# Performance work log

Measured on AMD Instinct MI355X. Metric: run time of the kernel, lower is better.

The kernel has to match this reference:

```python
import jax, jax.numpy as jnp
import numpy as np

R = 8
EPS = 1e-08


def diff_x(t, r):
    # t: (B,C,H,W), running cumsum along H -> windowed sum along H
    left = t[:, :, r:2 * r + 1]
    middle = t[:, :, 2 * r + 1:] - t[:, :, :-2 * r - 1]
    right = t[:, :, -1:] - t[:, :, -2 * r - 1:-r - 1]
    return jnp.concatenate([left, middle, right], axis=2)


def diff_y(t, r):
    left = t[:, :, :, r:2 * r + 1]
    middle = t[:, :, :, 2 * r + 1:] - t[:, :, :, :-2 * r - 1]
    right = t[:, :, :, -1:] - t[:, :, :, -2 * r - 1:-r - 1]
    return jnp.concatenate([left, middle, right], axis=3)


def box_filter(x, r):
    return diff_y(diff_x(jnp.cumsum(x, axis=2), r).cumsum(axis=3), r)


def bilinear_align_corners(x, H, W):
    # x: (B,C,h,w) -> (B,C,H,W), matching F.interpolate(mode='bilinear', align_corners=True)
    h, w = x.shape[2], x.shape[3]
    ys = jnp.linspace(0.0, h - 1.0, H, dtype=x.dtype)
    xs = jnp.linspace(0.0, w - 1.0, W, dtype=x.dtype)
    y0 = jnp.clip(jnp.floor(ys).astype(jnp.int32), 0, h - 1)
    x0 = jnp.clip(jnp.floor(xs).astype(jnp.int32), 0, w - 1)
    y1 = jnp.clip(y0 + 1, 0, h - 1)
    x1 = jnp.clip(x0 + 1, 0, w - 1)
    wy = (ys - y0.astype(x.dtype))[:, None]   # (H,1)
    wx = (xs - x0.astype(x.dtype))[None, :]   # (1,W)
    v00 = x[:, :, y0[:, None], x0[None, :]]
    v01 = x[:, :, y0[:, None], x1[None, :]]
    v10 = x[:, :, y1[:, None], x0[None, :]]
    v11 = x[:, :, y1[:, None], x1[None, :]]
    top = v00 * (1 - wx) + v01 * wx
    bot = v10 * (1 - wx) + v11 * wx
    return top * (1 - wy) + bot * wy


def setup_inputs() -> dict:
    key = jax.random.key(0)
    k1, k2, k3 = jax.random.split(key, 3)
    lr_x = jax.random.uniform(k1, (4, 3, 512, 512), dtype=jnp.float32)
    lr_y = jax.random.uniform(k2, (4, 3, 512, 512), dtype=jnp.float32)
    hr_x = jax.random.uniform(k3, (4, 3, 2048, 2048), dtype=jnp.float32)
    return {"lr_x": lr_x, "lr_y": lr_y, "hr_x": hr_x}


def reference(lr_x, lr_y, hr_x):
    _, _, h_lr, w_lr = lr_x.shape
    _, _, h_hr, w_hr = hr_x.shape
    N = box_filter(jnp.ones((1, 1, h_lr, w_lr), dtype=lr_x.dtype), R)
    mean_x = box_filter(lr_x, R) / N
    mean_y = box_filter(lr_y, R) / N
    cov_xy = box_filter(lr_x * lr_y, R) / N - mean_x * mean_y
    var_x = box_filter(lr_x * lr_x, R) / N - mean_x * mean_x
    A = cov_xy / (var_x + EPS)
    b = mean_y - A * mean_x
    mean_A = bilinear_align_corners(A, h_hr, w_hr)
    mean_b = bilinear_align_corners(b, h_hr, w_hr)
    return mean_A * hr_x + mean_b
```

## Files before the change

### kernel.cpp

```cpp
#include <hip/hip_runtime.h>

#define RR 8
#define TILE 32
#define EXT (TILE + 2 * RR)

__global__ __launch_bounds__(1024) void k_ab(
    const float* __restrict__ lrx, const float* __restrict__ lry,
    float* __restrict__ Aout, float* __restrict__ Bout, int H, int W) {
  __shared__ float sx[EXT][EXT];
  __shared__ float sy[EXT][EXT];
  __shared__ float hx[EXT][TILE];
  __shared__ float hy[EXT][TILE];
  __shared__ float hxy[EXT][TILE];
  __shared__ float hxx[EXT][TILE];

  const int bc = blockIdx.z;
  const size_t plane = (size_t)bc * H * W;
  const float* __restrict__ px = lrx + plane;
  const float* __restrict__ py = lry + plane;
  const int tx0 = blockIdx.x * TILE;
  const int ty0 = blockIdx.y * TILE;
  const int tid = threadIdx.y * TILE + threadIdx.x;

  for (int i = tid; i < EXT * EXT; i += TILE * TILE) {
    int r = i / EXT, c = i % EXT;
    int gy = ty0 + r - RR, gx = tx0 + c - RR;
    float vx = 0.f, vy = 0.f;
    if (gy >= 0 && gy < H && gx >= 0 && gx < W) {
      size_t o = (size_t)gy * W + gx;
      vx = px[o];
      vy = py[o];
    }
    sx[r][c] = vx;
    sy[r][c] = vy;
  }
  __syncthreads();

  for (int i = tid; i < EXT * TILE; i += TILE * TILE) {
    int r = i / TILE, c = i % TILE;
    float ax = 0.f, ay = 0.f, axy = 0.f, axx = 0.f;
#pragma unroll
    for (int d = 0; d <= 2 * RR; ++d) {
      float vx = sx[r][c + d];
      float vy = sy[r][c + d];
      ax += vx;
      ay += vy;
      axy += vx * vy;
      axx += vx * vx;
    }
    hx[r][c] = ax;
    hy[r][c] = ay;
    hxy[r][c] = axy;
    hxx[r][c] = axx;
  }
  __syncthreads();

  const int c = threadIdx.x, r = threadIdx.y;
  float sX = 0.f, sY = 0.f, sXY = 0.f, sXX = 0.f;
#pragma unroll
  for (int d = 0; d <= 2 * RR; ++d) {
    sX += hx[r + d][c];
    sY += hy[r + d][c];
    sXY += hxy[r + d][c];
    sXX += hxx[r + d][c];
  }
  const int gy = ty0 + r, gx = tx0 + c;
  if (gy < H && gx < W) {
    int ny = min(gy + RR, H - 1) - max(gy - RR, 0) + 1;
    int nx = min(gx + RR, W - 1) - max(gx - RR, 0) + 1;
    float inv = 1.f / (float)(nx * ny);
    float mx = sX * inv;
    float my = sY * inv;
    float cov = sXY * inv - mx * my;
    float var = sXX * inv - mx * mx;
    float a = cov / (var + 1e-8f);
    float bv = my - a * mx;
    size_t o = plane + (size_t)gy * W + gx;
    Aout[o] = a;
    Bout[o] = bv;
  }
}

__global__ __launch_bounds__(256) void k_out(
    const float* __restrict__ A, const float* __restrict__ Bb,
    const float* __restrict__ hr, float* __restrict__ out,
    int hl, int wl, int Hh, int Wh) {
  const int xq = blockIdx.x * blockDim.x + threadIdx.x;
  const int y = blockIdx.y;
  const int bc = blockIdx.z;

  const float scy = (float)(hl - 1) / (float)(Hh - 1);
  const float scx = (float)(wl - 1) / (float)(Wh - 1);

  float fy = (float)y * scy;
  int y0 = (int)fy;
  if (y0 > hl - 1) y0 = hl - 1;
  int y1 = y0 + 1;
  if (y1 > hl - 1) y1 = hl - 1;
  float wy = fy - (float)y0;

  const size_t lrBase = (size_t)bc * hl * wl;
  const float* __restrict__ A0 = A + lrBase + (size_t)y0 * wl;
  const float* __restrict__ A1 = A + lrBase + (size_t)y1 * wl;
  const float* __restrict__ B0 = Bb + lrBase + (size_t)y0 * wl;
  const float* __restrict__ B1 = Bb + lrBase + (size_t)y1 * wl;

  const size_t hrIdx = ((size_t)bc * Hh + y) * Wh + (size_t)xq * 4;
  const float4 h4 = *(const float4*)(hr + hrIdx);
  const float hv[4] = {h4.x, h4.y, h4.z, h4.w};
  float res[4];
  const int xg = xq * 4;
#pragma unroll
  for (int j = 0; j < 4; ++j) {
    float fx = (float)(xg + j) * scx;
    int x0 = (int)fx;
    if (x0 > wl - 1) x0 = wl - 1;
    int x1 = x0 + 1;
    if (x1 > wl - 1) x1 = wl - 1;
    float wx = fx - (float)x0;
    float a0 = A0[x0] + (A0[x1] - A0[x0]) * wx;
    float a1 = A1[x0] + (A1[x1] - A1[x0]) * wx;
    float av = a0 + (a1 - a0) * wy;
    float b0 = B0[x0] + (B0[x1] - B0[x0]) * wx;
    float b1 = B1[x0] + (B1[x1] - B1[x0]) * wx;
    float bv = b0 + (b1 - b0) * wy;
    res[j] = av * hv[j] + bv;
  }
  *(float4*)(out + hrIdx) = make_float4(res[0], res[1], res[2], res[3]);
}

extern "C" void kernel_launch(void* const* d_in, const int* in_sizes, int n_in,
                              void* d_out, int out_size, void* d_ws, size_t ws_size,
                              hipStream_t stream) {
  const float* lrx = (const float*)d_in[0];
  const float* lry = (const float*)d_in[1];
  const float* hrx = (const float*)d_in[2];
  float* out = (float*)d_out;

  const int BC = 12;
  const int hl = 512, wl = 512;
  const int Hh = 2048, Wh = 2048;

  float* A = (float*)d_ws;
  float* B = A + (size_t)BC * hl * wl;

  dim3 g1(wl / TILE, hl / TILE, BC);
  dim3 b1(TILE, TILE);
  k_ab<<<g1, b1, 0, stream>>>(lrx, lry, A, B, hl, wl);

  dim3 g2(Wh / 4 / 256, Hh, BC);
  dim3 b2(256);
  k_out<<<g2, b2, 0, stream>>>(A, B, hrx, out, hl, wl, Hh, Wh);
}
```

Baseline: 385.7 us.

## Register-blocked sliding-window box filter and LDS row interpolation for upsampling

The box-filter kernel now uses 256 threads, and each thread computes four outputs in both the horizontal and vertical passes. It loads values with float4 and updates a running window sum instead of re-summing all 17 taps. The output kernel first stages the y-interpolated A and b rows for each 1024-wide segment into LDS. It then does only x-interpolation from shared memory, which removes most of the redundant global gathers. Register use goes up, and an added LDS sync is the main risk; the output kernel is bandwidth-bound on hr_x and out regardless.

Result: faster. 371.7 us (-3.6%).

```diff
diff --git a/kernel.cpp b/kernel.cpp
--- a/kernel.cpp
+++ b/kernel.cpp
@@ -4,7 +4,7 @@
 #define TILE 32
 #define EXT (TILE + 2 * RR)
 
-__global__ __launch_bounds__(1024) void k_ab(
+__global__ __launch_bounds__(256) void k_ab(
     const float* __restrict__ lrx, const float* __restrict__ lry,
     float* __restrict__ Aout, float* __restrict__ Bout, int H, int W) {
   __shared__ float sx[EXT][EXT];
@@ -20,9 +20,9 @@
   const float* __restrict__ py = lry + plane;
   const int tx0 = blockIdx.x * TILE;
   const int ty0 = blockIdx.y * TILE;
-  const int tid = threadIdx.y * TILE + threadIdx.x;
+  const int tid = threadIdx.y * 32 + threadIdx.x;
 
-  for (int i = tid; i < EXT * EXT; i += TILE * TILE) {
+  for (int i = tid; i < EXT * EXT; i += 256) {
     int r = i / EXT, c = i % EXT;
     int gy = ty0 + r - RR, gx = tx0 + c - RR;
     float vx = 0.f, vy = 0.f;
@@ -36,38 +36,66 @@
   }
   __syncthreads();
 
-  for (int i = tid; i < EXT * TILE; i += TILE * TILE) {
-    int r = i / TILE, c = i % TILE;
+  for (int q = tid; q < EXT * (TILE / 4); q += 256) {
+    int r = q >> 3;
+    int c0 = (q & 7) * 4;
+    float xv[20], yv[20];
+#pragma unroll
+    for (int t = 0; t < 5; ++t) {
+      float4 x4 = *(const float4*)&sx[r][c0 + 4 * t];
+      float4 y4 = *(const float4*)&sy[r][c0 + 4 * t];
+      xv[4 * t + 0] = x4.x; xv[4 * t + 1] = x4.y; xv[4 * t + 2] = x4.z; xv[4 * t + 3] = x4.w;
+      yv[4 * t + 0] = y4.x; yv[4 * t + 1] = y4.y; yv[4 * t + 2] = y4.z; yv[4 * t + 3] = y4.w;
+    }
+    float pv[20], qv[20];
+#pragma unroll
+    for (int i = 0; i < 20; ++i) { pv[i] = xv[i] * yv[i]; qv[i] = xv[i] * xv[i]; }
     float ax = 0.f, ay = 0.f, axy = 0.f, axx = 0.f;
 #pragma unroll
-    for (int d = 0; d <= 2 * RR; ++d) {
-      float vx = sx[r][c + d];
-      float vy = sy[r][c + d];
-      ax += vx;
-      ay += vy;
-      axy += vx * vy;
-      axx += vx * vx;
+    for (int i = 0; i < 17; ++i) { ax += xv[i]; ay += yv[i]; axy += pv[i]; axx += qv[i]; }
+    float4 ox, oy, oxy, oxx;
+    ox.x = ax; oy.x = ay; oxy.x = axy; oxx.x = axx;
+#pragma unroll
+    for (int j = 1; j < 4; ++j) {
+      ax += xv[j + 16] - xv[j - 1];
+      ay += yv[j + 16] - yv[j - 1];
+      axy += pv[j + 16] - pv[j - 1];
+      axx += qv[j + 16] - qv[j - 1];
+      (&ox.x)[j] = ax; (&oy.x)[j] = ay; (&oxy.x)[j] = axy; (&oxx.x)[j] = axx;
     }
-    hx[r][c] = ax;
-    hy[r][c] = ay;
-    hxy[r][c] = axy;
-    hxx[r][c] = axx;
+    *(float4*)&hx[r][c0] = ox;
+    *(float4*)&hy[r][c0] = oy;
+    *(float4*)&hxy[r][c0] = oxy;
+    *(float4*)&hxx[r][c0] = oxx;
   }
   __syncthreads();
 
-  const int c = threadIdx.x, r = threadIdx.y;
+  const int c = threadIdx.x;
+  const int r0 = threadIdx.y * 4;
+  float vx[20], vy[20], vxy[20], vxx[20];
+#pragma unroll
+  for (int i = 0; i < 20; ++i) {
+    vx[i] = hx[r0 + i][c];
+    vy[i] = hy[r0 + i][c];
+    vxy[i] = hxy[r0 + i][c];
+    vxx[i] = hxx[r0 + i][c];
+  }
   float sX = 0.f, sY = 0.f, sXY = 0.f, sXX = 0.f;
 #pragma unroll
-  for (int d = 0; d <= 2 * RR; ++d) {
-    sX += hx[r + d][c];
-    sY += hy[r + d][c];
-    sXY += hxy[r + d][c];
-    sXX += hxx[r + d][c];
-  }
-  const int gy = ty0 + r, gx = tx0 + c;
-  if (gy < H && gx < W) {
-    int ny = min(gy + RR, H - 1) - max(gy - RR, 0) + 1;
-    int nx = min(gx + RR, W - 1) - max(gx - RR, 0) + 1;
+  for (int i = 0; i < 17; ++i) { sX += vx[i]; sY += vy[i]; sXY += vxy[i]; sXX += vxx[i]; }
+
+  const int gx = tx0 + c;
+  const int nx = min(gx + RR, W - 1) - max(gx - RR, 0) + 1;
+#pragma unroll
+  for (int j = 0; j < 4; ++j) {
+    if (j > 0) {
+      sX += vx[j + 16] - vx[j - 1];
+      sY += vy[j + 16] - vy[j - 1];
+      sXY += vxy[j + 16] - vxy[j - 1];
+      sXX += vxx[j + 16] - vxx[j - 1];
+    }
+    const int gy = ty0 + r0 + j;
+    const int ny = min(gy + RR, H - 1) - max(gy - RR, 0) + 1;
     float inv = 1.f / (float)(nx * ny);
     float mx = sX * inv;
     float my = sY * inv;
@@ -81,13 +109,17 @@
   }
 }
 
+#define KO_LDSW 264
 __global__ __launch_bounds__(256) void k_out(
     const float* __restrict__ A, const float* __restrict__ Bb,
     const float* __restrict__ hr, float* __restrict__ out,
     int hl, int wl, int Hh, int Wh) {
-  const int xq = blockIdx.x * blockDim.x + threadIdx.x;
+  __shared__ float Ay[KO_LDSW];
+  __shared__ float By[KO_LDSW];
+
   const int y = blockIdx.y;
   const int bc = blockIdx.z;
+  const int xb = blockIdx.x * 1024;
 
   const float scy = (float)(hl - 1) / (float)(Hh - 1);
   const float scx = (float)(wl - 1) / (float)(Wh - 1);
@@ -97,7 +129,11 @@
   if (y0 > hl - 1) y0 = hl - 1;
   int y1 = y0 + 1;
   if (y1 > hl - 1) y1 = hl - 1;
-  float wy = fy - (float)y0;
+  const float wy = fy - (float)y0;
+
+  const int x0base = (int)((float)xb * scx);
+  int x0max = (int)((float)(xb + 1023) * scx);
+  const int nW = x0max - x0base + 2;
 
   const size_t lrBase = (size_t)bc * hl * wl;
   const float* __restrict__ A0 = A + lrBase + (size_t)y0 * wl;
@@ -105,26 +141,30 @@
   const float* __restrict__ B0 = Bb + lrBase + (size_t)y0 * wl;
   const float* __restrict__ B1 = Bb + lrBase + (size_t)y1 * wl;
 
-  const size_t hrIdx = ((size_t)bc * Hh + y) * Wh + (size_t)xq * 4;
+  for (int i = threadIdx.x; i < nW; i += 256) {
+    int xl = x0base + i;
+    if (xl > wl - 1) xl = wl - 1;
+    float a0 = A0[xl], a1 = A1[xl];
+    float b0 = B0[xl], b1 = B1[xl];
+    Ay[i] = a0 + (a1 - a0) * wy;
+    By[i] = b0 + (b1 - b0) * wy;
+  }
+  __syncthreads();
+
+  const int xg = xb + threadIdx.x * 4;
+  const size_t hrIdx = ((size_t)bc * Hh + y) * Wh + xg;
   const float4 h4 = *(const float4*)(hr + hrIdx);
   const float hv[4] = {h4.x, h4.y, h4.z, h4.w};
   float res[4];
-  const int xg = xq * 4;
 #pragma unroll
   for (int j = 0; j < 4; ++j) {
     float fx = (float)(xg + j) * scx;
     int x0 = (int)fx;
-    if (x0 > wl - 1) x0 = wl - 1;
-    int x1 = x0 + 1;
-    if (x1 > wl - 1) x1 = wl - 1;
     float wx = fx - (float)x0;
-    float a0 = A0[x0] + (A0[x1] - A0[x0]) * wx;
-    float a1 = A1[x0] + (A1[x1] - A1[x0]) * wx;
-    float av = a0 + (a1 - a0) * wy;
-    float b0 = B0[x0] + (B0[x1] - B0[x0]) * wx;
-    float b1 = B1[x0] + (B1[x1] - B1[x0]) * wx;
-    float bv = b0 + (b1 - b0) * wy;
-    res[j] = av * hv[j] + bv;
+    int li = x0 - x0base;
+    float a = Ay[li] + (Ay[li + 1] - Ay[li]) * wx;
+    float b = By[li] + (By[li + 1] - By[li]) * wx;
+    res[j] = a * hv[j] + b;
   }
   *(float4*)(out + hrIdx) = make_float4(res[0], res[1], res[2], res[3]);
 }
@@ -145,10 +185,10 @@
   float* B = A + (size_t)BC * hl * wl;
 
   dim3 g1(wl / TILE, hl / TILE, BC);
-  dim3 b1(TILE, TILE);
+  dim3 b1(32, 8);
   k_ab<<<g1, b1, 0, stream>>>(lrx, lry, A, B, hl, wl);
 
-  dim3 g2(Wh / 4 / 256, Hh, BC);
+  dim3 g2(Wh / 1024, Hh, BC);
   dim3 b2(256);
   k_out<<<g2, b2, 0, stream>>>(A, B, hrx, out, hl, wl, Hh, Wh);
 }
```

## Fuse guided-filter coefficient computation into the upsample kernel with halo recompute

Applied to the files above, without the earlier changes.

Replaces the two-kernel pipeline (compute A/b to workspace, then bilinear-upsample and apply) with a single kernel. Each block recomputes the low-res A and b rows it needs, using sliding-window box sums held in registers and LDS, then interpolates and writes a 4x512 output tile. This removes the workspace round-trip, the second launch and the scattered global gathers of A/b. In exchange, each block redundantly recomputes halo regions, runs serial prologue phases with block barriers, and uses roughly 55KB of LDS, which limits how many blocks can be resident per CU while streaming the high-res input.

Result: slower. 607.0 us (+57.4%).

```diff
diff --git a/kernel.cpp b/kernel.cpp
--- a/kernel.cpp
+++ b/kernel.cpp
@@ -1,132 +1,146 @@
 #include <hip/hip_runtime.h>
 
-#define RR 8
-#define TILE 32
-#define EXT (TILE + 2 * RR)
+#define AW 132
 
-__global__ __launch_bounds__(1024) void k_ab(
+__global__ __launch_bounds__(256) void k_fused(
     const float* __restrict__ lrx, const float* __restrict__ lry,
-    float* __restrict__ Aout, float* __restrict__ Bout, int H, int W) {
-  __shared__ float sx[EXT][EXT];
-  __shared__ float sy[EXT][EXT];
-  __shared__ float hx[EXT][TILE];
-  __shared__ float hy[EXT][TILE];
-  __shared__ float hxy[EXT][TILE];
-  __shared__ float hxx[EXT][TILE];
+    const float* __restrict__ hr, float* __restrict__ out) {
+  const int hl = 512, wl = 512, Hh = 2048, Wh = 2048;
+
+  __shared__ float hX[19][AW], hY[19][AW], hXY[19][AW], hXX[19][AW];
+  __shared__ float AL[3][AW], bL[3][AW];
+  __shared__ float Ay[4][AW], By[4][AW];
 
   const int bc = blockIdx.z;
-  const size_t plane = (size_t)bc * H * W;
+  const int yb = blockIdx.y * 4;
+  const int xb = blockIdx.x * 512;
+  const int tid = threadIdx.x;
+
+  const float sc = 511.f / 2047.f;
+
+  const int x0base = (int)((float)xb * sc);
+  const int x0max = (int)((float)(xb + 511) * sc);
+  const int nW = x0max - x0base + 2;
+  const int ylo = (int)((float)yb * sc);
+  int yhi = (int)((float)(yb + 3) * sc) + 1;
+  if (yhi > hl - 1) yhi = hl - 1;
+  const int NR = yhi - ylo + 1;
+
+  const size_t plane = (size_t)bc * hl * wl;
   const float* __restrict__ px = lrx + plane;
   const float* __restrict__ py = lry + plane;
-  const int tx0 = blockIdx.x * TILE;
-  const int ty0 = blockIdx.y * TILE;
-  const int tid = threadIdx.y * TILE + threadIdx.x;
 
-  for (int i = tid; i < EXT * EXT; i += TILE * TILE) {
-    int r = i / EXT, c = i % EXT;
-    int gy = ty0 + r - RR, gx = tx0 + c - RR;
-    float vx = 0.f, vy = 0.f;
-    if (gy >= 0 && gy < H && gx >= 0 && gx < W) {
-      size_t o = (size_t)gy * W + gx;
-      vx = px[o];
-      vy = py[o];
+  if (tid < 171) {
+    const int rr = tid / 9;
+    const int g = tid - rr * 9;
+    const int yr = ylo - 8 + rr;
+    float X[32], Y[32];
+    if (yr >= 0 && yr < hl) {
+      const float* __restrict__ rx = px + (size_t)yr * wl;
+      const float* __restrict__ ry = py + (size_t)yr * wl;
+      const int gx0 = x0base - 8 + 16 * g;
+#pragma unroll
+      for (int k = 0; k < 32; ++k) {
+        int gx = gx0 + k;
+        bool in = (gx >= 0 && gx < wl);
+        X[k] = in ? rx[gx] : 0.f;
+        Y[k] = in ? ry[gx] : 0.f;
+      }
+    } else {
+#pragma unroll
+      for (int k = 0; k < 32; ++k) { X[k] = 0.f; Y[k] = 0.f; }
     }
-    sx[r][c] = vx;
-    sy[r][c] = vy;
+    float sX = 0.f, sY = 0.f, sXY = 0.f, sXX = 0.f;
+#pragma unroll
+    for (int k = 0; k < 17; ++k) {
+      sX += X[k]; sY += Y[k]; sXY += X[k] * Y[k]; sXX += X[k] * X[k];
+    }
+#pragma unroll
+    for (int j = 0; j < 16; ++j) {
+      if (j > 0) {
+        sX += X[j + 16] - X[j - 1];
+        sY += Y[j + 16] - Y[j - 1];
+        sXY += X[j + 16] * Y[j + 16] - X[j - 1] * Y[j - 1];
+        sXX += X[j + 16] * X[j + 16] - X[j - 1] * X[j - 1];
+      }
+      int L = 16 * g + j;
+      if (L < nW) {
+        hX[rr][L] = sX; hY[rr][L] = sY; hXY[rr][L] = sXY; hXX[rr][L] = sXX;
+      }
+    }
   }
   __syncthreads();
 
-  for (int i = tid; i < EXT * TILE; i += TILE * TILE) {
-    int r = i / TILE, c = i % TILE;
-    float ax = 0.f, ay = 0.f, axy = 0.f, axx = 0.f;
+  if (tid < nW) {
+    const int c = tid;
+    float sX = 0.f, sY = 0.f, sXY = 0.f, sXX = 0.f;
 #pragma unroll
-    for (int d = 0; d <= 2 * RR; ++d) {
-      float vx = sx[r][c + d];
-      float vy = sy[r][c + d];
-      ax += vx;
-      ay += vy;
-      axy += vx * vy;
-      axx += vx * vx;
+    for (int k = 0; k < 17; ++k) {
+      sX += hX[k][c]; sY += hY[k][c]; sXY += hXY[k][c]; sXX += hXX[k][c];
     }
-    hx[r][c] = ax;
-    hy[r][c] = ay;
-    hxy[r][c] = axy;
-    hxx[r][c] = axx;
+    const int gx = x0base + c;
+    const int nx = min(gx + 8, wl - 1) - max(gx - 8, 0) + 1;
+    for (int ri = 0; ri < NR; ++ri) {
+      if (ri > 0) {
+        sX += hX[ri + 16][c] - hX[ri - 1][c];
+        sY += hY[ri + 16][c] - hY[ri - 1][c];
+        sXY += hXY[ri + 16][c] - hXY[ri - 1][c];
+        sXX += hXX[ri + 16][c] - hXX[ri - 1][c];
+      }
+      const int r = ylo + ri;
+      const int ny = min(r + 8, hl - 1) - max(r - 8, 0) + 1;
+      float inv = 1.f / (float)(nx * ny);
+      float mx = sX * inv;
+      float my = sY * inv;
+      float cov = sXY * inv - mx * my;
+      float var = sXX * inv - mx * mx;
+      float a = cov / (var + 1e-8f);
+      AL[ri][c] = a;
+      bL[ri][c] = my - a * mx;
+    }
   }
   __syncthreads();
 
-  const int c = threadIdx.x, r = threadIdx.y;
-  float sX = 0.f, sY = 0.f, sXY = 0.f, sXX = 0.f;
 #pragma unroll
-  for (int d = 0; d <= 2 * RR; ++d) {
-    sX += hx[r + d][c];
-    sY += hy[r + d][c];
-    sXY += hxy[r + d][c];
-    sXX += hxx[r + d][c];
+  for (int rr = 0; rr < 4; ++rr) {
+    float fy = (float)(yb + rr) * sc;
+    int y0 = (int)fy;
+    if (y0 > hl - 1) y0 = hl - 1;
+    int y1 = y0 + 1;
+    if (y1 > hl - 1) y1 = hl - 1;
+    float wy = fy - (float)y0;
+    int l0 = y0 - ylo, l1 = y1 - ylo;
+    if (tid < nW) {
+      float a0 = AL[l0][tid], a1 = AL[l1][tid];
+      float b0 = bL[l0][tid], b1 = bL[l1][tid];
+      Ay[rr][tid] = a0 + (a1 - a0) * wy;
+      By[rr][tid] = b0 + (b1 - b0) * wy;
+    }
   }
-  const int gy = ty0 + r, gx = tx0 + c;
-  if (gy < H && gx < W) {
-    int ny = min(gy + RR, H - 1) - max(gy - RR, 0) + 1;
-    int nx = min(gx + RR, W - 1) - max(gx - RR, 0) + 1;
-    float inv = 1.f / (float)(nx * ny);
-    float mx = sX * inv;
-    float my = sY * inv;
-    float cov = sXY * inv - mx * my;
-    float var = sXX * inv - mx * mx;
-    float a = cov / (var + 1e-8f);
-    float bv = my - a * mx;
-    size_t o = plane + (size_t)gy * W + gx;
-    Aout[o] = a;
-    Bout[o] = bv;
+  __syncthreads();
+
+  const size_t hrPlane = (size_t)bc * Hh * Wh;
+#pragma unroll
+  for (int k = 0; k < 2; ++k) {
+    const int idx = tid + 256 * k;
+    const int rr = idx >> 7;
+    const int c4 = idx & 127;
+    const int xg = xb + c4 * 4;
+    const size_t o = hrPlane + (size_t)(yb + rr) * Wh + xg;
+    const float4 h4 = *(const float4*)(hr + o);
+    float4 o4;
+#pragma unroll
+    for (int j = 0; j < 4; ++j) {
+      float fx = (float)(xg + j) * sc;
+      int x0 = (int)fx;
+      float wx = fx - (float)x0;
+      int li = x0 - x0base;
+      float a = Ay[rr][li] + (Ay[rr][li + 1] - Ay[rr][li]) * wx;
+      float b = By[rr][li] + (By[rr][li + 1] - By[rr][li]) * wx;
+      (&o4.x)[j] = a * (&h4.x)[j] + b;
+    }
+    *(float4*)(out + o) = o4;
   }
-}
-
-__global__ __launch_bounds__(256) void k_out(
-    const float* __restrict__ A, const float* __restrict__ Bb,
-    const float* __restrict__ hr, float* __restrict__ out,
-    int hl, int wl, int Hh, int Wh) {
-  const int xq = blockIdx.x * blockDim.x + threadIdx.x;
-  const int y = blockIdx.y;
-  const int bc = blockIdx.z;
-
-  const float scy = (float)(hl - 1) / (float)(Hh - 1);
-  const float scx = (float)(wl - 1) / (float)(Wh - 1);
-
-  float fy = (float)y * scy;
-  int y0 = (int)fy;
-  if (y0 > hl - 1) y0 = hl - 1;
-  int y1 = y0 + 1;
-  if (y1 > hl - 1) y1 = hl - 1;
-  float wy = fy - (float)y0;
-
-  const size_t lrBase = (size_t)bc * hl * wl;
-  const float* __restrict__ A0 = A + lrBase + (size_t)y0 * wl;
-  const float* __restrict__ A1 = A + lrBase + (size_t)y1 * wl;
-  const float* __restrict__ B0 = Bb + lrBase + (size_t)y0 * wl;
-  const float* __restrict__ B1 = Bb + lrBase + (size_t)y1 * wl;
-
-  const size_t hrIdx = ((size_t)bc * Hh + y) * Wh + (size_t)xq * 4;
-  const float4 h4 = *(const float4*)(hr + hrIdx);
-  const float hv[4] = {h4.x, h4.y, h4.z, h4.w};
-  float res[4];
-  const int xg = xq * 4;
-#pragma unroll
-  for (int j = 0; j < 4; ++j) {
-    float fx = (float)(xg + j) * scx;
-    int x0 = (int)fx;
-    if (x0 > wl - 1) x0 = wl - 1;
-    int x1 = x0 + 1;
-    if (x1 > wl - 1) x1 = wl - 1;
-    float wx = fx - (float)x0;
-    float a0 = A0[x0] + (A0[x1] - A0[x0]) * wx;
-    float a1 = A1[x0] + (A1[x1] - A1[x0]) * wx;
-    float av = a0 + (a1 - a0) * wy;
-    float b0 = B0[x0] + (B0[x1] - B0[x0]) * wx;
-    float b1 = B1[x0] + (B1[x1] - B1[x0]) * wx;
-    float bv = b0 + (b1 - b0) * wy;
-    res[j] = av * hv[j] + bv;
-  }
-  *(float4*)(out + hrIdx) = make_float4(res[0], res[1], res[2], res[3]);
 }
 
 extern "C" void kernel_launch(void* const* d_in, const int* in_sizes, int n_in,
@@ -137,18 +151,7 @@
   const float* hrx = (const float*)d_in[2];
   float* out = (float*)d_out;
 
-  const int BC = 12;
-  const int hl = 512, wl = 512;
-  const int Hh = 2048, Wh = 2048;
-
-  float* A = (float*)d_ws;
-  float* B = A + (size_t)BC * hl * wl;
-
-  dim3 g1(wl / TILE, hl / TILE, BC);
-  dim3 b1(TILE, TILE);
-  k_ab<<<g1, b1, 0, stream>>>(lrx, lry, A, B, hl, wl);
-
-  dim3 g2(Wh / 4 / 256, Hh, BC);
-  dim3 b2(256);
-  k_out<<<g2, b2, 0, stream>>>(A, B, hrx, out, hl, wl, Hh, Wh);
+  dim3 grid(2048 / 512, 2048 / 4, 12);
+  dim3 block(256);
+  k_fused<<<grid, block, 0, stream>>>(lrx, lry, hrx, out);
 }
```
